# Performance work log

Measured on AMD Instinct MI355X. Metric: run time of the kernel, lower is better.

The kernel has to match this reference:

```python
import jax, jax.numpy as jnp
import numpy as np

B, S, D, H = 4, 2048, 512, 8

def setup_inputs() -> dict:
    key = jax.random.key(0)
    ks = jax.random.split(key, 6)
    query = jax.random.normal(ks[0], (B, S, D), dtype=jnp.float32)
    value = jax.random.normal(ks[1], (B, S, D), dtype=jnp.float32)
    # causal additive mask, broadcast over heads: [H, S, S]
    causal = jnp.where(jnp.tril(jnp.ones((S, S), dtype=bool)), 0.0, -1e9).astype(jnp.float32)
    mask = jnp.broadcast_to(causal[None, :, :], (H, S, S))
    sd = 1.0 / np.sqrt(D)
    Wq = jax.random.normal(ks[2], (D, D), dtype=jnp.float32) * sd
    Wkv = jax.random.normal(ks[3], (D, 2 * D), dtype=jnp.float32) * sd
    Wo = jax.random.normal(ks[4], (D, D), dtype=jnp.float32) * sd
    normalizer = jnp.asarray(1.0 / np.sqrt(D // H), dtype=jnp.float32)  # 1/sqrt(head_size)
    head_mults = jnp.ones((1, 1, H, 1), dtype=jnp.float32)
    return {"query": query, "value": value, "mask": mask, "Wq": Wq, "Wkv": Wkv,
            "Wo": Wo, "normalizer": normalizer, "head_mults": head_mults}

def reference(query, value, mask, Wq, Wkv, Wo, normalizer, head_mults):
    b, sq, d = query.shape
    h = head_mults.shape[2]
    q = (query @ Wq).reshape(b, sq, h, -1)                 # [b,q,h,hd]
    k, v = jnp.split(value @ Wkv, 2, axis=-1)
    sk = value.shape[1]
    k = k.reshape(b, sk, h, -1)
    v = v.reshape(b, sk, h, -1)
    score = jnp.einsum('bqhd,bkhd->bhqk', q, k) * normalizer
    score = score + mask[None, :, :, :]
    align = jax.nn.softmax(score, axis=-1)
    heads = jnp.einsum('bhqk,bkhd->bqhd', align, v)        # [b,q,h,hd]
    # cross-head normalization (over head axis, ddof=0 like tf.reduce_std)
    mean = jnp.mean(heads, axis=-2, keepdims=True)
    std = jnp.std(heads, axis=-2, keepdims=True)
    heads = (heads - mean) / (std + 0.01)
    heads = heads * head_mults
    out = heads.reshape(b, sq, d) @ Wo
    return out
```

## Files before the change

### kernel.cpp

```cpp
#include <hip/hip_runtime.h>


typedef float  f32x4  __attribute__((ext_vector_type(4)));
typedef __bf16 bf16x8 __attribute__((ext_vector_type(8)));
typedef short  s16x4  __attribute__((ext_vector_type(4)));
typedef unsigned short u16;

#define BS 2048
#define DD 512
#define NH 8
#define NQ (4 * BS * DD)

__device__ __forceinline__ u16 f2bf(float f) {
  union { float f; unsigned u; } v; v.f = f;
  unsigned r = v.u + 0x7fffu + ((v.u >> 16) & 1u);
  return (u16)(r >> 16);
}

__device__ __forceinline__ void gll16(const u16* g, u16* l) {
  __builtin_amdgcn_global_load_lds((const __attribute__((address_space(1))) void*)g,
                                   (__attribute__((address_space(3))) void*)l, 16, 0, 0);
}

#if defined(__has_builtin)
#if __has_builtin(__builtin_amdgcn_mfma_f32_16x16x16bf16_1k)
#define HAVE_1K 1
#endif
#endif
__device__ __forceinline__ f32x4 mfma_pv(s16x4 a, s16x4 b, f32x4 c) {
#ifdef HAVE_1K
  return __builtin_amdgcn_mfma_f32_16x16x16bf16_1k(a, b, c, 0, 0, 0);
#else
  bf16x8 a8 = {}, b8 = {};
  s16x4* ap = (s16x4*)&a8; s16x4* bp = (s16x4*)&b8;
  ap[0] = a; bp[0] = b;
  return __builtin_amdgcn_mfma_f32_16x16x32_bf16(a8, b8, c, 0, 0, 0);
#endif
}


__global__ __launch_bounds__(256) void cvt2(const float* __restrict__ q,
                                            const float* __restrict__ v,
                                            u16* __restrict__ qb, u16* __restrict__ vb) {
  int i = (blockIdx.x * 256 + threadIdx.x) * 4;
  const float* s; u16* d;
  if (i < NQ) { s = q + i; d = qb + i; }
  else        { s = v + (i - NQ); d = vb + (i - NQ); }
  float4 x = *(const float4*)s;
  ushort4 o; o.x = f2bf(x.x); o.y = f2bf(x.y); o.z = f2bf(x.z); o.w = f2bf(x.w);
  *(ushort4*)d = o;
}

__global__ __launch_bounds__(256) void wtrans_all(const float* __restrict__ Wq,
                                                  const float* __restrict__ Wkv,
                                                  const float* __restrict__ Wo,
                                                  u16* __restrict__ WqT,
                                                  u16* __restrict__ WkvT,
                                                  u16* __restrict__ WoT) {
  int i = blockIdx.x * 256 + threadIdx.x;
  if (i < 262144) {
    int n = i >> 9, k = i & 511;
    WqT[i] = f2bf(Wq[k * 512 + n]);
  } else if (i < 786432) {
    int j = i - 262144; int n = j >> 9, k = j & 511;
    WkvT[j] = f2bf(Wkv[k * 1024 + n]);
  } else {
    int j = i - 786432; int n = j >> 9, k = j & 511;
    WoT[j] = f2bf(Wo[k * 512 + n]);
  }
}


__device__ __forceinline__ void gemm_core(const u16* __restrict__ A,
                                          const u16* __restrict__ Bt,
                                          int m0, int n0, int K,
                                          u16* Al, u16* Bl, f32x4 acc[4][4]) {
  const int t = threadIdx.x;
  const int wv = t >> 6, ln = t & 63, qd = ln >> 4, l16 = ln & 15;
  const int rw = (wv & 1) * 64, cw = (wv >> 1) * 64;
  const int sr = wv * 16 + (ln >> 2), sc = (ln & 3) * 8;
  for (int k0 = 0; k0 < K; k0 += 32) {
    __syncthreads();
#pragma unroll
    for (int c = 0; c < 2; ++c) {
      int r = c * 64 + sr;
      gll16(&A[(long)(m0 + r) * K + k0 + sc], &Al[r * 32 + sc]);
      gll16(&Bt[(long)(n0 + r) * K + k0 + sc], &Bl[r * 32 + sc]);
    }
    __syncthreads();
    bf16x8 af[4], bfr[4];
#pragma unroll
    for (int i = 0; i < 4; ++i) af[i] = *(const bf16x8*)&Al[(rw + i * 16 + l16) * 32 + qd * 8];
#pragma unroll
    for (int j = 0; j < 4; ++j) bfr[j] = *(const bf16x8*)&Bl[(cw + j * 16 + l16) * 32 + qd * 8];
#pragma unroll
    for (int i = 0; i < 4; ++i)
#pragma unroll
      for (int j = 0; j < 4; ++j)
        acc[i][j] = __builtin_amdgcn_mfma_f32_16x16x32_bf16(af[i], bfr[j], acc[i][j], 0, 0, 0);
  }
}

__global__ __launch_bounds__(256) void qkv_gemm(const u16* __restrict__ qA,
                                                const u16* __restrict__ vA,
                                                const u16* __restrict__ WqT,
                                                const u16* __restrict__ WkvT,
                                                u16* __restrict__ Qb,
                                                u16* __restrict__ Kb,
                                                u16* __restrict__ Vt) {
  __shared__ __align__(16) u16 Al[128 * 32];
  __shared__ __align__(16) u16 Bl[128 * 32];
  const bool isQ = blockIdx.y < 4;
  const u16* A = isQ ? qA : vA;
  const u16* Bt = isQ ? WqT : WkvT;
  const int n0 = (isQ ? blockIdx.y : blockIdx.y - 4) * 128;
  const int m0 = blockIdx.x * 128;
  f32x4 acc[4][4] = {};
  gemm_core(A, Bt, m0, n0, 512, Al, Bl, acc);
  const int t = threadIdx.x;
  const int wv = t >> 6, ln = t & 63, qd = ln >> 4, l16 = ln & 15;
  const int rw = (wv & 1) * 64, cw = (wv >> 1) * 64;
  if (isQ) {
#pragma unroll
    for (int i = 0; i < 4; ++i)
#pragma unroll
      for (int j = 0; j < 4; ++j) {
        int row = m0 + rw + i * 16 + qd * 4, col = n0 + cw + j * 16 + l16;
#pragma unroll
        for (int r = 0; r < 4; ++r)
          Qb[(long)(row + r) * 512 + col] = f2bf(acc[i][j][r]);
      }
  } else {
#pragma unroll
    for (int j = 0; j < 4; ++j) {
      int col = n0 + cw + j * 16 + l16;
      if (col < 512) {
#pragma unroll
        for (int i = 0; i < 4; ++i) {
          int row = m0 + rw + i * 16 + qd * 4;
#pragma unroll
          for (int r = 0; r < 4; ++r)
            Kb[(long)(row + r) * 512 + col] = f2bf(acc[i][j][r]);
        }
      } else {
        int c2 = col - 512, hh = c2 >> 6, dd = c2 & 63;
#pragma unroll
        for (int i = 0; i < 4; ++i) {
          int sg = m0 + rw + i * 16 + qd * 4;
          int bb = sg >> 11, ss = sg & 2047;
          ushort4 o;
          o.x = f2bf(acc[i][j][0]); o.y = f2bf(acc[i][j][1]);
          o.z = f2bf(acc[i][j][2]); o.w = f2bf(acc[i][j][3]);
          *(ushort4*)&Vt[((long)(bb * 8 + hh) * 64 + dd) * 2048 + ss] = o;
        }
      }
    }
  }
}

__global__ __launch_bounds__(256) void out_gemm(const u16* __restrict__ A,
                                                const u16* __restrict__ Bt,
                                                float* __restrict__ C) {
  __shared__ __align__(16) u16 Al[128 * 32];
  __shared__ __align__(16) u16 Bl[128 * 32];
  const int m0 = blockIdx.x * 128, n0 = blockIdx.y * 128;
  f32x4 acc[4][4] = {};
  gemm_core(A, Bt, m0, n0, 512, Al, Bl, acc);
  const int t = threadIdx.x;
  const int wv = t >> 6, ln = t & 63, qd = ln >> 4, l16 = ln & 15;
  const int rw = (wv & 1) * 64, cw = (wv >> 1) * 64;
#pragma unroll
  for (int i = 0; i < 4; ++i)
#pragma unroll
    for (int j = 0; j < 4; ++j) {
      int row = m0 + rw + i * 16 + qd * 4, col = n0 + cw + j * 16 + l16;
#pragma unroll
      for (int r = 0; r < 4; ++r)
        C[(long)(row + r) * 512 + col] = acc[i][j][r];
    }
}

__global__ __launch_bounds__(256) void attn(const u16* __restrict__ Qb,
                                            const u16* __restrict__ Kb,
                                            const u16* __restrict__ Vt,
                                            float* __restrict__ heads,
                                            const float* __restrict__ normp) {
  constexpr int ST = 72;
  __shared__ __align__(16) u16 Qs[64 * ST], Ks[64 * ST], Vts[64 * ST];
  const float scale = normp[0];
  const int t = threadIdx.x;
  const int wv = t >> 6, ln = t & 63, qd = ln >> 4, l16 = ln & 15;
  const int sr = t >> 2, scg = (t & 3) * 16;
  const int h = blockIdx.y, b = blockIdx.z;
  const int bs0 = b * BS;
  const u16* vtb = Vt + ((long)(b * 8 + h) * 64) * 2048;

  for (int qsel = 0; qsel < 2; ++qsel) {
    const int qt = qsel ? (31 - (int)blockIdx.x) : (int)blockIdx.x;
    __syncthreads();
    {
      const u16* src = &Qb[(long)(bs0 + qt * 64 + sr) * 512 + h * 64 + scg];
      *(bf16x8*)&Qs[sr * ST + scg] = *(const bf16x8*)src;
      *(bf16x8*)&Qs[sr * ST + scg + 8] = *(const bf16x8*)(src + 8);
    }
    float m_i = -1e30f, l_i = 0.f;
    f32x4 o[4] = {};

    for (int kb = 0; kb <= qt; ++kb) {
      __syncthreads();
      {
        const u16* ksrc = &Kb[(long)(bs0 + kb * 64 + sr) * 512 + h * 64 + scg];
        *(bf16x8*)&Ks[sr * ST + scg] = *(const bf16x8*)ksrc;
        *(bf16x8*)&Ks[sr * ST + scg + 8] = *(const bf16x8*)(ksrc + 8);
        const u16* vsrc = &vtb[(long)sr * 2048 + kb * 64 + scg];
        *(bf16x8*)&Vts[sr * ST + scg] = *(const bf16x8*)vsrc;
        *(bf16x8*)&Vts[sr * ST + scg + 8] = *(const bf16x8*)(vsrc + 8);
      }
      __syncthreads();

      f32x4 s[4] = {};
#pragma unroll
      for (int c = 0; c < 2; ++c) {
        bf16x8 bq = *(const bf16x8*)&Qs[(wv * 16 + l16) * ST + c * 32 + qd * 8];
#pragma unroll
        for (int nt = 0; nt < 4; ++nt) {
          bf16x8 ak = *(const bf16x8*)&Ks[(nt * 16 + l16) * ST + c * 32 + qd * 8];
          s[nt] = __builtin_amdgcn_mfma_f32_16x16x32_bf16(ak, bq, s[nt], 0, 0, 0);
        }
      }

      const int limi = (kb == qt) ? (wv * 16 + l16) : 1 << 20;
      float mx = -1e30f;
#pragma unroll
      for (int nt = 0; nt < 4; ++nt)
#pragma unroll
        for (int r = 0; r < 4; ++r) {
          float v = s[nt][r] * scale;
          if (nt * 16 + qd * 4 + r > limi) v = -1e30f;
          s[nt][r] = v;
          mx = fmaxf(mx, v);
        }
      mx = fmaxf(mx, __shfl_xor(mx, 16));
      mx = fmaxf(mx, __shfl_xor(mx, 32));
      float mn = fmaxf(m_i, mx);
      float al = __expf(m_i - mn);
      float rs = 0.f;
#pragma unroll
      for (int nt = 0; nt < 4; ++nt)
#pragma unroll
        for (int r = 0; r < 4; ++r) {
          float p = __expf(s[nt][r] - mn);
          s[nt][r] = p;
          rs += p;
        }
      rs += __shfl_xor(rs, 16);
      rs += __shfl_xor(rs, 32);
      l_i = l_i * al + rs;
      m_i = mn;
#pragma unroll
      for (int n2 = 0; n2 < 4; ++n2) o[n2] *= al;

      s16x4 pf[4];
#pragma unroll
      for (int c2 = 0; c2 < 4; ++c2)
#pragma unroll
        for (int j = 0; j < 4; ++j) pf[c2][j] = (short)f2bf(s[c2][j]);

#pragma unroll
      for (int n2 = 0; n2 < 4; ++n2)
#pragma unroll
        for (int c2 = 0; c2 < 4; ++c2) {
          s16x4 av = *(const s16x4*)&Vts[(n2 * 16 + l16) * ST + c2 * 16 + qd * 4];
          o[n2] = mfma_pv(av, pf[c2], o[n2]);
        }
    }

    float inv = 1.f / l_i;
    float* dst = &heads[(long)(bs0 + qt * 64 + wv * 16 + l16) * DD + h * 64 + qd * 4];
#pragma unroll
    for (int n2 = 0; n2 < 4; ++n2)
      *(f32x4*)(dst + n2 * 16) = o[n2] * inv;
  }
}

__global__ __launch_bounds__(256) void headnorm(const float* __restrict__ heads,
                                                const float* __restrict__ hm,
                                                u16* __restrict__ outn) {
  int i = blockIdx.x * 256 + threadIdx.x;
  int d = i & 63, bs = i >> 6;
  const float* p = heads + (long)bs * DD + d;
  float x[NH], mean = 0.f;
#pragma unroll
  for (int h = 0; h < NH; ++h) { x[h] = p[h * 64]; mean += x[h]; }
  mean *= 0.125f;
  float var = 0.f;
#pragma unroll
  for (int h = 0; h < NH; ++h) { float dd = x[h] - mean; var += dd * dd; }
  var *= 0.125f;
  float inv = 1.f / (sqrtf(var) + 0.01f);
#pragma unroll
  for (int h = 0; h < NH; ++h)
    outn[(long)bs * DD + h * 64 + d] = f2bf((x[h] - mean) * inv * hm[h]);
}

extern "C" void kernel_launch(void* const* d_in, const int* in_sizes, int n_in,
                              void* d_out, int out_size, void* d_ws, size_t ws_size,
                              hipStream_t stream) {
  const float* query = (const float*)d_in[0];
  const float* value = (const float*)d_in[1];
  const float* Wq    = (const float*)d_in[3];
  const float* Wkv   = (const float*)d_in[4];
  const float* Wo    = (const float*)d_in[5];
  const float* normp = (const float*)d_in[6];
  const float* hmult = (const float*)d_in[7];

  char* ws = (char*)d_ws;
  const size_t MB = 1 << 20;
  u16*   qbf   = (u16*)(ws);
  u16*   vbf   = (u16*)(ws + 8 * MB);
  u16*   WqT   = (u16*)(ws + 16 * MB);
  u16*   WkvT  = (u16*)(ws + 16 * MB + 524288);
  u16*   WoT   = (u16*)(ws + 17 * MB + 524288);
  u16*   Qb    = (u16*)(ws + 18 * MB);
  u16*   Kb    = (u16*)(ws + 26 * MB);
  u16*   Vt    = (u16*)(ws + 34 * MB);
  float* heads = (float*)(ws + 42 * MB);
  u16*   hN    = (u16*)(ws + 58 * MB);

  cvt2<<<2 * NQ / 4 / 256, 256, 0, stream>>>(query, value, qbf, vbf);
  wtrans_all<<<1048576 / 256, 256, 0, stream>>>(Wq, Wkv, Wo, WqT, WkvT, WoT);
  qkv_gemm<<<dim3(64, 12), 256, 0, stream>>>(qbf, vbf, WqT, WkvT, Qb, Kb, Vt);
  attn<<<dim3(16, NH, 4), 256, 0, stream>>>(Qb, Kb, Vt, heads, normp);
  headnorm<<<(4 * BS * 64) / 256, 256, 0, stream>>>(heads, hmult, hN);
  out_gemm<<<dim3(64, 4), 256, 0, stream>>>(hN, WoT, (float*)d_out);
}
```

Before: 317.9 us.

## Fuse prep kernels, tile weight transpose, prefetch K/V, emit bf16 heads, use exp2

Merges the input conversion and weight transpose into one launch, and rewrites the transpose to go through a shared-memory tile so global reads and writes are coalesced. The attention loop now loads the next K/V tile into registers while computing on the current one. Softmax uses exp2 with the log2(e) factor folded into the scale. Attention output is written as bf16 staged through LDS for coalesced stores, which halves headnorm's read traffic but adds one more bf16 rounding before the cross-head normalization.

```diff
diff --git a/kernel.cpp b/kernel.cpp
--- a/kernel.cpp
+++ b/kernel.cpp
@@ -15,6 +15,9 @@
   union { float f; unsigned u; } v; v.f = f;
   unsigned r = v.u + 0x7fffu + ((v.u >> 16) & 1u);
   return (u16)(r >> 16);
+}
+__device__ __forceinline__ float bf2f(u16 b) {
+  union { unsigned u; float f; } v; v.u = ((unsigned)b) << 16; return v.f;
 }
 
 __device__ __forceinline__ void gll16(const u16* g, u16* l) {
@@ -32,44 +35,56 @@
   return __builtin_amdgcn_mfma_f32_16x16x16bf16_1k(a, b, c, 0, 0, 0);
 #else
   bf16x8 a8 = {}, b8 = {};
-  s16x4* ap = (s16x4*)&a8; s16x4* bp = (s16x4*)&b8;
-  ap[0] = a; bp[0] = b;
+  *(s16x4*)&a8 = a; *(s16x4*)&b8 = b;
   return __builtin_amdgcn_mfma_f32_16x16x32_bf16(a8, b8, c, 0, 0, 0);
 #endif
 }
 
-
-__global__ __launch_bounds__(256) void cvt2(const float* __restrict__ q,
+__global__ __launch_bounds__(256) void prep(const float* __restrict__ q,
                                             const float* __restrict__ v,
-                                            u16* __restrict__ qb, u16* __restrict__ vb) {
-  int i = (blockIdx.x * 256 + threadIdx.x) * 4;
-  const float* s; u16* d;
-  if (i < NQ) { s = q + i; d = qb + i; }
-  else        { s = v + (i - NQ); d = vb + (i - NQ); }
-  float4 x = *(const float4*)s;
-  ushort4 o; o.x = f2bf(x.x); o.y = f2bf(x.y); o.z = f2bf(x.z); o.w = f2bf(x.w);
-  *(ushort4*)d = o;
-}
-
-__global__ __launch_bounds__(256) void wtrans_all(const float* __restrict__ Wq,
-                                                  const float* __restrict__ Wkv,
-                                                  const float* __restrict__ Wo,
-                                                  u16* __restrict__ WqT,
-                                                  u16* __restrict__ WkvT,
-                                                  u16* __restrict__ WoT) {
-  int i = blockIdx.x * 256 + threadIdx.x;
-  if (i < 262144) {
-    int n = i >> 9, k = i & 511;
-    WqT[i] = f2bf(Wq[k * 512 + n]);
-  } else if (i < 786432) {
-    int j = i - 262144; int n = j >> 9, k = j & 511;
-    WkvT[j] = f2bf(Wkv[k * 1024 + n]);
-  } else {
-    int j = i - 786432; int n = j >> 9, k = j & 511;
-    WoT[j] = f2bf(Wo[k * 512 + n]);
-  }
-}
-
+                                            const float* __restrict__ Wq,
+                                            const float* __restrict__ Wkv,
+                                            const float* __restrict__ Wo,
+                                            u16* __restrict__ qb, u16* __restrict__ vb,
+                                            u16* __restrict__ WqT, u16* __restrict__ WkvT,
+                                            u16* __restrict__ WoT) {
+  __shared__ float Ts[64][65];
+  const int t = threadIdx.x;
+  int bx = blockIdx.x;
+  if (bx < 8192) {
+    int i = (bx * 256 + t) * 4;
+    const float* s; u16* d;
+    if (i < NQ) { s = q + i; d = qb + i; }
+    else        { s = v + (i - NQ); d = vb + (i - NQ); }
+    float4 x = *(const float4*)s;
+    ushort4 o; o.x = f2bf(x.x); o.y = f2bf(x.y); o.z = f2bf(x.z); o.w = f2bf(x.w);
+    *(ushort4*)d = o;
+    return;
+  }
+  int tb = bx - 8192;
+  const float* W; u16* Wt; int N, ntn;
+  if (tb < 64)       { W = Wq;  Wt = WqT;  N = 512;  ntn = 8; }
+  else if (tb < 192) { W = Wkv; Wt = WkvT; N = 1024; ntn = 16; tb -= 64; }
+  else               { W = Wo;  Wt = WoT;  N = 512;  ntn = 8;  tb -= 192; }
+  int tk = tb / ntn, tn = tb - tk * ntn;
+  int r = t >> 2, c0 = (t & 3) * 16;
+  const float* src = &W[(long)(tk * 64 + r) * N + tn * 64 + c0];
+#pragma unroll
+  for (int j = 0; j < 4; ++j) {
+    float4 x = *(const float4*)(src + j * 4);
+    Ts[r][c0 + j * 4 + 0] = x.x; Ts[r][c0 + j * 4 + 1] = x.y;
+    Ts[r][c0 + j * 4 + 2] = x.z; Ts[r][c0 + j * 4 + 3] = x.w;
+  }
+  __syncthreads();
+  u16* dst = &Wt[(long)(tn * 64 + r) * 512 + tk * 64 + c0];
+#pragma unroll
+  for (int m = 0; m < 4; ++m) {
+    ushort4 o;
+    o.x = f2bf(Ts[c0 + m * 4 + 0][r]); o.y = f2bf(Ts[c0 + m * 4 + 1][r]);
+    o.z = f2bf(Ts[c0 + m * 4 + 2][r]); o.w = f2bf(Ts[c0 + m * 4 + 3][r]);
+    *(ushort4*)(dst + m * 4) = o;
+  }
+}
 
 __device__ __forceinline__ void gemm_core(const u16* __restrict__ A,
                                           const u16* __restrict__ Bt,
@@ -183,11 +198,11 @@
 __global__ __launch_bounds__(256) void attn(const u16* __restrict__ Qb,
                                             const u16* __restrict__ Kb,
                                             const u16* __restrict__ Vt,
-                                            float* __restrict__ heads,
+                                            u16* __restrict__ heads,
                                             const float* __restrict__ normp) {
   constexpr int ST = 72;
   __shared__ __align__(16) u16 Qs[64 * ST], Ks[64 * ST], Vts[64 * ST];
-  const float scale = normp[0];
+  const float scale2 = normp[0] * 1.44269504f;
   const int t = threadIdx.x;
   const int wv = t >> 6, ln = t & 63, qd = ln >> 4, l16 = ln & 15;
   const int sr = t >> 2, scg = (t & 3) * 16;
@@ -203,20 +218,24 @@
       *(bf16x8*)&Qs[sr * ST + scg] = *(const bf16x8*)src;
       *(bf16x8*)&Qs[sr * ST + scg + 8] = *(const bf16x8*)(src + 8);
     }
+    bf16x8 kr0, kr1, vr0, vr1;
+#define FETCH(KB) do { \
+      const u16* kp_ = &Kb[(long)(bs0 + (KB) * 64 + sr) * 512 + h * 64 + scg]; \
+      kr0 = *(const bf16x8*)kp_; kr1 = *(const bf16x8*)(kp_ + 8); \
+      const u16* vp_ = &vtb[(long)sr * 2048 + (KB) * 64 + scg]; \
+      vr0 = *(const bf16x8*)vp_; vr1 = *(const bf16x8*)(vp_ + 8); } while (0)
+    FETCH(0);
     float m_i = -1e30f, l_i = 0.f;
     f32x4 o[4] = {};
 
     for (int kb = 0; kb <= qt; ++kb) {
       __syncthreads();
-      {
-        const u16* ksrc = &Kb[(long)(bs0 + kb * 64 + sr) * 512 + h * 64 + scg];
-        *(bf16x8*)&Ks[sr * ST + scg] = *(const bf16x8*)ksrc;
-        *(bf16x8*)&Ks[sr * ST + scg + 8] = *(const bf16x8*)(ksrc + 8);
-        const u16* vsrc = &vtb[(long)sr * 2048 + kb * 64 + scg];
-        *(bf16x8*)&Vts[sr * ST + scg] = *(const bf16x8*)vsrc;
-        *(bf16x8*)&Vts[sr * ST + scg + 8] = *(const bf16x8*)(vsrc + 8);
-      }
+      *(bf16x8*)&Ks[sr * ST + scg] = kr0;
+      *(bf16x8*)&Ks[sr * ST + scg + 8] = kr1;
+      *(bf16x8*)&Vts[sr * ST + scg] = vr0;
+      *(bf16x8*)&Vts[sr * ST + scg + 8] = vr1;
       __syncthreads();
+      if (kb < qt) FETCH(kb + 1);
 
       f32x4 s[4] = {};
 #pragma unroll
@@ -235,7 +254,7 @@
       for (int nt = 0; nt < 4; ++nt)
 #pragma unroll
         for (int r = 0; r < 4; ++r) {
-          float v = s[nt][r] * scale;
+          float v = s[nt][r] * scale2;
           if (nt * 16 + qd * 4 + r > limi) v = -1e30f;
           s[nt][r] = v;
           mx = fmaxf(mx, v);
@@ -243,13 +262,13 @@
       mx = fmaxf(mx, __shfl_xor(mx, 16));
       mx = fmaxf(mx, __shfl_xor(mx, 32));
       float mn = fmaxf(m_i, mx);
-      float al = __expf(m_i - mn);
+      float al = exp2f(m_i - mn);
       float rs = 0.f;
 #pragma unroll
       for (int nt = 0; nt < 4; ++nt)
 #pragma unroll
         for (int r = 0; r < 4; ++r) {
-          float p = __expf(s[nt][r] - mn);
+          float p = exp2f(s[nt][r] - mn);
           s[nt][r] = p;
           rs += p;
         }
@@ -274,24 +293,33 @@
           o[n2] = mfma_pv(av, pf[c2], o[n2]);
         }
     }
+#undef FETCH
 
     float inv = 1.f / l_i;
-    float* dst = &heads[(long)(bs0 + qt * 64 + wv * 16 + l16) * DD + h * 64 + qd * 4];
+    __syncthreads();
 #pragma unroll
     for (int n2 = 0; n2 < 4; ++n2)
-      *(f32x4*)(dst + n2 * 16) = o[n2] * inv;
-  }
-}
-
-__global__ __launch_bounds__(256) void headnorm(const float* __restrict__ heads,
+#pragma unroll
+      for (int r = 0; r < 4; ++r)
+        Ks[(wv * 16 + l16) * ST + n2 * 16 + qd * 4 + r] = f2bf(o[n2][r] * inv);
+    __syncthreads();
+    {
+      u16* dst = &heads[(long)(bs0 + qt * 64 + sr) * 512 + h * 64 + scg];
+      *(bf16x8*)dst = *(const bf16x8*)&Ks[sr * ST + scg];
+      *(bf16x8*)(dst + 8) = *(const bf16x8*)&Ks[sr * ST + scg + 8];
+    }
+  }
+}
+
+__global__ __launch_bounds__(256) void headnorm(const u16* __restrict__ heads,
                                                 const float* __restrict__ hm,
                                                 u16* __restrict__ outn) {
   int i = blockIdx.x * 256 + threadIdx.x;
   int d = i & 63, bs = i >> 6;
-  const float* p = heads + (long)bs * DD + d;
+  const u16* p = heads + (long)bs * DD + d;
   float x[NH], mean = 0.f;
 #pragma unroll
-  for (int h = 0; h < NH; ++h) { x[h] = p[h * 64]; mean += x[h]; }
+  for (int h = 0; h < NH; ++h) { x[h] = bf2f(p[h * 64]); mean += x[h]; }
   mean *= 0.125f;
   float var = 0.f;
 #pragma unroll
@@ -324,11 +352,11 @@
   u16*   Qb    = (u16*)(ws + 18 * MB);
   u16*   Kb    = (u16*)(ws + 26 * MB);
   u16*   Vt    = (u16*)(ws + 34 * MB);
-  float* heads = (float*)(ws + 42 * MB);
-  u16*   hN    = (u16*)(ws + 58 * MB);
-
-  cvt2<<<2 * NQ / 4 / 256, 256, 0, stream>>>(query, value, qbf, vbf);
-  wtrans_all<<<1048576 / 256, 256, 0, stream>>>(Wq, Wkv, Wo, WqT, WkvT, WoT);
+  u16*   heads = (u16*)(ws + 42 * MB);
+  u16*   hN    = (u16*)(ws + 50 * MB);
+
+  prep<<<8448, 256, 0, stream>>>(query, value, Wq, Wkv, Wo,
+                                 qbf, vbf, WqT, WkvT, WoT);
   qkv_gemm<<<dim3(64, 12), 256, 0, stream>>>(qbf, vbf, WqT, WkvT, Qb, Kb, Vt);
   attn<<<dim3(16, NH, 4), 256, 0, stream>>>(Qb, Kb, Vt, heads, normp);
   headnorm<<<(4 * BS * 64) / 256, 256, 0, stream>>>(heads, hmult, hN);
```

Result: faster. 302.9 us (-4.7%).
